# Optimization experiments

Measured on AMD Instinct MI355X. Metric: run time of the kernel, lower is better.

The kernel has to match this reference:

```python
import jax, jax.numpy as jnp
import numpy as np

B, S, H, NH, HD = 2, 2048, 2048, 32, 64
ROPE_THETA = 10000.0


def _rope_tables(seq_len, head_dim, theta):
    inv_freq = 1.0 / (theta ** (jnp.arange(0, head_dim, 2, dtype=jnp.float32) / head_dim))
    t = jnp.arange(seq_len, dtype=jnp.float32)
    freqs = jnp.outer(t, inv_freq)                 # [S, HD/2]
    emb = jnp.concatenate([freqs, freqs], axis=-1)  # [S, HD]
    return jnp.cos(emb), jnp.sin(emb)


def setup_inputs() -> dict:
    key = jax.random.key(0)
    ks = jax.random.split(key, 6)
    cos, sin = _rope_tables(S, HD, ROPE_THETA)
    scale = 0.02
    return {
        "hidden_states": jax.random.normal(ks[0], (B, S, H), dtype=jnp.float32),
        "attention_mask": jnp.zeros((B, S), dtype=jnp.float32),
        "cos": cos,
        "sin": sin,
        "Wq": jax.random.normal(ks[1], (H, H), dtype=jnp.float32) * scale,
        "Wk": jax.random.normal(ks[2], (H, H), dtype=jnp.float32) * scale,
        "Wv": jax.random.normal(ks[3], (H, H), dtype=jnp.float32) * scale,
        "Wo": jax.random.normal(ks[4], (H, H), dtype=jnp.float32) * scale,
    }


def _rotate_half(x):
    x1, x2 = jnp.split(x, 2, axis=-1)
    return jnp.concatenate([-x2, x1], axis=-1)


def reference(hidden_states, attention_mask, cos, sin, Wq, Wk, Wv, Wo):
    b, s, _ = hidden_states.shape
    # QKV projections (nn.Linear: x @ W.T), reshape to [B, NH, S, HD]
    def proj(W):
        y = hidden_states @ W.T
        return y.reshape(b, s, NH, HD).transpose(0, 2, 1, 3)
    q, k, v = proj(Wq), proj(Wk), proj(Wv)
    # RoPE (HF rotate_half convention); cos/sin: [S, HD] -> broadcast [1,1,S,HD]
    c = cos[None, None, :, :]
    sn = sin[None, None, :, :]
    q = q * c + _rotate_half(q) * sn
    k = k * c + _rotate_half(k) * sn
    # attention: [B, NH, S, S]
    scores = jnp.einsum("bhqd,bhkd->bhqk", q, k) / jnp.sqrt(jnp.float32(HD))
    scores = scores + attention_mask[:, None, None, :]
    probs = jax.nn.softmax(scores, axis=-1)
    out = jnp.einsum("bhqk,bhkd->bhqd", probs, v)
    out = out.transpose(0, 2, 1, 3).reshape(b, s, NH * HD)
    return out @ Wo.T
```

## Files before the change

kernel.cpp:

```cpp
#include <hip/hip_runtime.h>
#include <stdint.h>
#include <math.h>

#define NB 2
#define SS 2048
#define HH 2048
#define NHH 32
#define HDD 64
#define MM (NB*SS)

typedef __attribute__((ext_vector_type(8))) short short8;
typedef __attribute__((ext_vector_type(4))) short short4v;
typedef __attribute__((ext_vector_type(4))) float f32x4;

#define GLOBAL_AS const __attribute__((address_space(1))) void*
#define LDS_AS __attribute__((address_space(3))) void*

static __device__ __forceinline__ short rne_bf16(float x) {
    uint32_t u = __builtin_bit_cast(uint32_t, x);
    u += 0x7FFFu + ((u >> 16) & 1u);
    return (short)(u >> 16);
}
static __device__ __forceinline__ float bf16f(short h) {
    return __builtin_bit_cast(float, (uint32_t)((uint16_t)h) << 16);
}
static __device__ __forceinline__ uint32_t pack_bf16_rne(float a, float b) {
    uint32_t ua = __builtin_bit_cast(uint32_t, a);
    uint32_t ub = __builtin_bit_cast(uint32_t, b);
    ua += 0x7FFFu + ((ua >> 16) & 1u);
    ub += 0x7FFFu + ((ub >> 16) & 1u);
    return __builtin_amdgcn_perm(ub, ua, 0x07060302);
}
static __device__ __forceinline__ float fast_exp2(float x) {
    float r;
    asm("v_exp_f32 %0, %1" : "=v"(r) : "v"(x));
    return r;
}

__global__ void __launch_bounds__(256)
k_cvt(const float* __restrict__ in, short* __restrict__ out, int n4) {
    int i = blockIdx.x * blockDim.x + threadIdx.x;
    if (i >= n4) return;
    float4 f = reinterpret_cast<const float4*>(in)[i];
    short4v o;
    o.x = rne_bf16(f.x); o.y = rne_bf16(f.y);
    o.z = rne_bf16(f.z); o.w = rne_bf16(f.w);
    reinterpret_cast<short4v*>(out)[i] = o;
}

__global__ void __launch_bounds__(256)
k_cvt_split(const float* __restrict__ in, short* __restrict__ hi, short* __restrict__ lo, int n4) {
    int i = blockIdx.x * blockDim.x + threadIdx.x;
    if (i >= n4) return;
    float4 f = reinterpret_cast<const float4*>(in)[i];
    short4v h, l;
    h.x = rne_bf16(f.x); l.x = rne_bf16(f.x - bf16f(h.x));
    h.y = rne_bf16(f.y); l.y = rne_bf16(f.y - bf16f(h.y));
    h.z = rne_bf16(f.z); l.z = rne_bf16(f.z - bf16f(h.z));
    h.w = rne_bf16(f.w); l.w = rne_bf16(f.w - bf16f(h.w));
    reinterpret_cast<short4v*>(hi)[i] = h;
    reinterpret_cast<short4v*>(lo)[i] = l;
}

__global__ void __launch_bounds__(256, 2)
k_gemm_qkv(const short* __restrict__ X,
           const short* __restrict__ Wqh, const short* __restrict__ Wkh, const short* __restrict__ Wvh,
           const float* __restrict__ cosT, const float* __restrict__ sinT,
           short* __restrict__ Qr, short* __restrict__ Kr, short* __restrict__ Vt)
{
    __shared__ short lA[128 * 32];
    __shared__ short lBq[128 * 32];
    __shared__ short lBk[128 * 32];
    __shared__ short lBv[128 * 32];
    const int tid = threadIdx.x;
    const int lane = tid & 63;
    const int wave = tid >> 6;
    const int lrow = lane & 15;
    const int quad = lane >> 4;
    const int mblk = blockIdx.y * 128;
    const int nblk = blockIdx.x * 128;
    const int m0 = mblk + (wave >> 1) * 64;
    const int n0 = nblk + (wave & 1) * 64;
    const int mw = (wave >> 1) * 64;
    const int nw = (wave & 1) * 64;

    const int srow = wave * 32 + (lane >> 2);
    const int skc = (lane & 3) * 8;
    const short* gA = X   + (size_t)(mblk + srow) * HH + skc;
    const short* gQ = Wqh + (size_t)(nblk + srow) * HH + skc;
    const short* gK = Wkh + (size_t)(nblk + srow) * HH + skc;
    const short* gV = Wvh + (size_t)(nblk + srow) * HH + skc;
    const int lofs = wave * 1024;

    f32x4 acc[3][4][4];
    #pragma unroll
    for (int z = 0; z < 3; z++)
        #pragma unroll
        for (int i = 0; i < 4; i++)
            #pragma unroll
            for (int j = 0; j < 4; j++) acc[z][i][j] = 0.f;

    #pragma unroll 1
    for (int k0 = 0; k0 < HH; k0 += 32) {
        __syncthreads();
        #pragma unroll
        for (int j = 0; j < 2; j++) {
            size_t go = (size_t)j * 16 * HH + k0;
            int lo = lofs + j * 512;
            __builtin_amdgcn_global_load_lds((GLOBAL_AS)(gA + go), (LDS_AS)(&lA[lo]),  16, 0, 0);
            __builtin_amdgcn_global_load_lds((GLOBAL_AS)(gQ + go), (LDS_AS)(&lBq[lo]), 16, 0, 0);
            __builtin_amdgcn_global_load_lds((GLOBAL_AS)(gK + go), (LDS_AS)(&lBk[lo]), 16, 0, 0);
            __builtin_amdgcn_global_load_lds((GLOBAL_AS)(gV + go), (LDS_AS)(&lBv[lo]), 16, 0, 0);
        }
        __syncthreads();

        short8 a[4];
        #pragma unroll
        for (int mt = 0; mt < 4; mt++)
            a[mt] = *reinterpret_cast<const short8*>(&lA[(mw + mt * 16 + lrow) * 32 + quad * 8]);

        const short* lBz[3] = { lBq, lBk, lBv };
        #pragma unroll
        for (int z = 0; z < 3; z++) {
            short8 b[4];
            #pragma unroll
            for (int nt = 0; nt < 4; nt++)
                b[nt] = *reinterpret_cast<const short8*>(&lBz[z][(nw + nt * 16 + lrow) * 32 + quad * 8]);
            #pragma unroll
            for (int mt = 0; mt < 4; mt++)
                #pragma unroll
                for (int nt = 0; nt < 4; nt++)
                    acc[z][mt][nt] = __builtin_amdgcn_mfma_f32_16x16x32_bf16(a[mt], b[nt], acc[z][mt][nt], 0, 0, 0);
        }
    }

    const float QSCL = 0.18033688011112042f;

    #pragma unroll
    for (int z = 0; z < 3; z++) {
        #pragma unroll
        for (int mt = 0; mt < 4; mt++) {
            #pragma unroll
            for (int r = 0; r < 4; r++) {
                int row = m0 + mt * 16 + quad * 4 + r;
                int b_i = row >> 11;
                int s_i = row & (SS - 1);
                #pragma unroll
                for (int nt = 0; nt < 4; nt++) {
                    int col = n0 + nt * 16 + lrow;
                    int h_i = col >> 6;
                    int d_i = col & 63;
                    float v = acc[z][mt][nt][r];
                    if (z < 2) {
                        float pair = (nt & 2) ? acc[z][mt][nt - 2][r] : -acc[z][mt][nt + 2][r];
                        float c = cosT[s_i * HDD + d_i];
                        float sn = sinT[s_i * HDD + d_i];
                        v = v * c + pair * sn;
                        if (z == 0) v *= QSCL;
                        short* dst = (z == 0) ? Qr : Kr;
                        dst[(((size_t)b_i * NHH + h_i) * SS + s_i) * HDD + d_i] = rne_bf16(v);
                    } else {
                        Vt[(((size_t)b_i * NHH + h_i) * HDD + d_i) * SS + s_i] = rne_bf16(v);
                    }
                }
            }
        }
    }
}

__global__ void __launch_bounds__(256, 2)
k_attn(const short* __restrict__ Qr, const short* __restrict__ Kr, const short* __restrict__ Vt,
       const float* __restrict__ mask,
       short* __restrict__ Ah, short* __restrict__ Al)
{
    __shared__ short plds[4][4096];
    const int lane = threadIdx.x & 63;
    const int wave = threadIdx.x >> 6;
    const int lrow = lane & 15;
    const int quad = lane >> 4;
    const int aofs = lrow & 7;
    const int b = blockIdx.x >> 5;
    const int h = blockIdx.x & 31;
    const int q0w = blockIdx.y * 256 + wave * 64;

    const size_t bh = (size_t)b * NHH + h;
    const short* Qbase = Qr + bh * SS * HDD;
    const short* Kbase = Kr + bh * SS * HDD;
    const short* Vbase = Vt + bh * (size_t)HDD * SS;
    const float* mrow = mask + b * SS;
    char* cb = (char*)&plds[wave][0];

    short8 qf[4][2];
    #pragma unroll
    for (int nt = 0; nt < 4; nt++)
        #pragma unroll
        for (int c = 0; c < 2; c++)
            qf[nt][c] = *reinterpret_cast<const short8*>(
                Qbase + (size_t)(q0w + nt * 16 + lrow) * HDD + c * 32 + quad * 8);

    f32x4 oacc[4][4];
    float l[4];
    #pragma unroll
    for (int i = 0; i < 4; i++) {
        l[i] = 0.f;
        #pragma unroll
        for (int j = 0; j < 4; j++) oacc[i][j] = 0.f;
    }

    const float L2E = 1.44269504f;

    #pragma unroll 1
    for (int k0 = 0; k0 < SS; k0 += 64) {
        short8 kf[4][2];
        #pragma unroll
        for (int kt = 0; kt < 4; kt++)
            #pragma unroll
            for (int c = 0; c < 2; c++)
                kf[kt][c] = *reinterpret_cast<const short8*>(
                    Kbase + (size_t)(k0 + kt * 16 + lrow) * HDD + c * 32 + quad * 8);

        f32x4 sacc[4][4];
        #pragma unroll
        for (int kt = 0; kt < 4; kt++)
            #pragma unroll
            for (int nt = 0; nt < 4; nt++) {
                f32x4 z4 = 0.f;
                z4 = __builtin_amdgcn_mfma_f32_16x16x32_bf16(kf[kt][0], qf[nt][0], z4, 0, 0, 0);
                sacc[kt][nt] = __builtin_amdgcn_mfma_f32_16x16x32_bf16(kf[kt][1], qf[nt][1], z4, 0, 0, 0);
            }

        asm volatile("s_waitcnt lgkmcnt(0)" ::: "memory");

        #pragma unroll
        for (int kt = 0; kt < 4; kt++) {
            float4 mk = *reinterpret_cast<const float4*>(mrow + k0 + kt * 16 + quad * 4);
            float m0v = mk.x * L2E, m1v = mk.y * L2E, m2v = mk.z * L2E, m3v = mk.w * L2E;
            #pragma unroll
            for (int nt = 0; nt < 4; nt++) {
                float p0 = fast_exp2(sacc[kt][nt][0] + m0v);
                float p1 = fast_exp2(sacc[kt][nt][1] + m1v);
                float p2 = fast_exp2(sacc[kt][nt][2] + m2v);
                float p3 = fast_exp2(sacc[kt][nt][3] + m3v);
                l[nt] += (p0 + p1) + (p2 + p3);
                uint2 w;
                w.x = pack_bf16_rne(p0, p1);
                w.y = pack_bf16_rne(p2, p3);
                *reinterpret_cast<uint2*>(
                    cb + (nt * 16 + lrow) * 128 +
                    (((2 * kt + (quad >> 1)) ^ aofs) * 16) + (quad & 1) * 8) = w;
            }
        }

        asm volatile("s_waitcnt lgkmcnt(0)" ::: "memory");

        #pragma unroll
        for (int c = 0; c < 2; c++) {
            short8 pf[4], vf[4];
            #pragma unroll
            for (int mt = 0; mt < 4; mt++)
                pf[mt] = *reinterpret_cast<const short8*>(
                    cb + (mt * 16 + lrow) * 128 + (((4 * c + quad) ^ aofs) * 16));
            #pragma unroll
            for (int dt = 0; dt < 4; dt++)
                vf[dt] = *reinterpret_cast<const short8*>(
                    Vbase + (size_t)(dt * 16 + lrow) * SS + k0 + c * 32 + quad * 8);
            #pragma unroll
            for (int mt = 0; mt < 4; mt++)
                #pragma unroll
                for (int dt = 0; dt < 4; dt++)
                    oacc[mt][dt] = __builtin_amdgcn_mfma_f32_16x16x32_bf16(pf[mt], vf[dt], oacc[mt][dt], 0, 0, 0);
        }
    }

    #pragma unroll
    for (int nt = 0; nt < 4; nt++) {
        l[nt] += __shfl_xor(l[nt], 16, 64);
        l[nt] += __shfl_xor(l[nt], 32, 64);
    }
    float linv[4][4];
    #pragma unroll
    for (int mt = 0; mt < 4; mt++)
        #pragma unroll
        for (int r = 0; r < 4; r++)
            linv[mt][r] = 1.f / __shfl(l[mt], quad * 4 + r, 16);

    #pragma unroll
    for (int mt = 0; mt < 4; mt++) {
        #pragma unroll
        for (int r = 0; r < 4; r++) {
            int s_i = q0w + mt * 16 + quad * 4 + r;
            size_t row = (size_t)b * SS + s_i;
            #pragma unroll
            for (int dt = 0; dt < 4; dt++) {
                float x = oacc[mt][dt][r] * linv[mt][r];
                short hi = rne_bf16(x);
                short lo = rne_bf16(x - bf16f(hi));
                size_t idx = row * HH + (size_t)h * 64 + dt * 16 + lrow;
                Ah[idx] = hi;
                Al[idx] = lo;
            }
        }
    }
}

__global__ void __launch_bounds__(256, 2)
k_gemm_wo(const short* __restrict__ Ahh, const short* __restrict__ All,
          const short* __restrict__ Bhh, const short* __restrict__ Bll,
          float* __restrict__ C)
{
    __shared__ short lAh[128 * 32];
    __shared__ short lAl[128 * 32];
    __shared__ short lBh[128 * 32];
    __shared__ short lBl[128 * 32];
    const int tid = threadIdx.x;
    const int lane = tid & 63;
    const int wave = tid >> 6;
    const int lrow = lane & 15;
    const int quad = lane >> 4;
    const int mblk = blockIdx.y * 128;
    const int nblk = blockIdx.x * 128;
    const int m0 = mblk + (wave >> 1) * 64;
    const int n0 = nblk + (wave & 1) * 64;
    const int mw = (wave >> 1) * 64;
    const int nw = (wave & 1) * 64;

    const int srow = wave * 32 + (lane >> 2);
    const int skc = (lane & 3) * 8;
    const short* gAh = Ahh + (size_t)(mblk + srow) * HH + skc;
    const short* gAl = All + (size_t)(mblk + srow) * HH + skc;
    const short* gBh = Bhh + (size_t)(nblk + srow) * HH + skc;
    const short* gBl = Bll + (size_t)(nblk + srow) * HH + skc;
    short* lAhw = &lAh[wave * 1024];
    short* lAlw = &lAl[wave * 1024];
    short* lBhw = &lBh[wave * 1024];
    short* lBlw = &lBl[wave * 1024];

    f32x4 acc[4][4];
    #pragma unroll
    for (int i = 0; i < 4; i++)
        #pragma unroll
        for (int j = 0; j < 4; j++) acc[i][j] = 0.f;

    #pragma unroll 1
    for (int k0 = 0; k0 < HH; k0 += 32) {
        __syncthreads();
        #pragma unroll
        for (int j = 0; j < 2; j++) {
            size_t go = (size_t)j * 16 * HH + k0;
            __builtin_amdgcn_global_load_lds((GLOBAL_AS)(gAh + go), (LDS_AS)(lAhw + j * 512), 16, 0, 0);
            __builtin_amdgcn_global_load_lds((GLOBAL_AS)(gAl + go), (LDS_AS)(lAlw + j * 512), 16, 0, 0);
            __builtin_amdgcn_global_load_lds((GLOBAL_AS)(gBh + go), (LDS_AS)(lBhw + j * 512), 16, 0, 0);
            __builtin_amdgcn_global_load_lds((GLOBAL_AS)(gBl + go), (LDS_AS)(lBlw + j * 512), 16, 0, 0);
        }
        __syncthreads();

        short8 ah[4], al[4], bh[4], bl[4];
        #pragma unroll
        for (int mt = 0; mt < 4; mt++) {
            int off = (mw + mt * 16 + lrow) * 32 + quad * 8;
            ah[mt] = *reinterpret_cast<const short8*>(&lAh[off]);
            al[mt] = *reinterpret_cast<const short8*>(&lAl[off]);
        }
        #pragma unroll
        for (int nt = 0; nt < 4; nt++) {
            int off = (nw + nt * 16 + lrow) * 32 + quad * 8;
            bh[nt] = *reinterpret_cast<const short8*>(&lBh[off]);
            bl[nt] = *reinterpret_cast<const short8*>(&lBl[off]);
        }
        #pragma unroll
        for (int mt = 0; mt < 4; mt++)
            #pragma unroll
            for (int nt = 0; nt < 4; nt++) {
                acc[mt][nt] = __builtin_amdgcn_mfma_f32_16x16x32_bf16(ah[mt], bh[nt], acc[mt][nt], 0, 0, 0);
                acc[mt][nt] = __builtin_amdgcn_mfma_f32_16x16x32_bf16(al[mt], bh[nt], acc[mt][nt], 0, 0, 0);
                acc[mt][nt] = __builtin_amdgcn_mfma_f32_16x16x32_bf16(ah[mt], bl[nt], acc[mt][nt], 0, 0, 0);
            }
    }

    #pragma unroll
    for (int mt = 0; mt < 4; mt++)
        #pragma unroll
        for (int r = 0; r < 4; r++) {
            int row = m0 + mt * 16 + quad * 4 + r;
            #pragma unroll
            for (int nt = 0; nt < 4; nt++) {
                int col = n0 + nt * 16 + lrow;
                C[(size_t)row * HH + col] = acc[mt][nt][r];
            }
        }
}

extern "C" void kernel_launch(void* const* d_in, const int* in_sizes, int n_in,
                              void* d_out, int out_size, void* d_ws, size_t ws_size,
                              hipStream_t stream) {
    const float* hidden = (const float*)d_in[0];
    const float* maskp  = (const float*)d_in[1];
    const float* cosT   = (const float*)d_in[2];
    const float* sinT   = (const float*)d_in[3];
    const float* Wq     = (const float*)d_in[4];
    const float* Wk     = (const float*)d_in[5];
    const float* Wv     = (const float*)d_in[6];
    const float* Wo     = (const float*)d_in[7];
    float* out = (float*)d_out;

    char* ws = (char*)d_ws;
    auto alloc = [&](size_t bytes) {
        char* p = ws;
        ws += (bytes + 255) & ~(size_t)255;
        return p;
    };
    const size_t XB = (size_t)MM * HH * sizeof(short);
    const size_t WB = (size_t)HH * HH * sizeof(short);
    short* Xh  = (short*)alloc(XB);
    short* Wqh = (short*)alloc(WB);
    short* Wkh = (short*)alloc(WB);
    short* Wvh = (short*)alloc(WB);
    short* Woh = (short*)alloc(WB);
    short* Wol = (short*)alloc(WB);
    short* Qr  = (short*)alloc(XB);
    short* Kr  = (short*)alloc(XB);
    short* Vt  = (short*)alloc(XB);
    short* Ah  = (short*)alloc(XB);
    short* Al  = (short*)alloc(XB);

    const int nX4 = MM * HH / 4;
    const int nW4 = HH * HH / 4;
    k_cvt<<<dim3(nX4 / 256), dim3(256), 0, stream>>>(hidden, Xh, nX4);
    k_cvt<<<dim3(nW4 / 256), dim3(256), 0, stream>>>(Wq, Wqh, nW4);
    k_cvt<<<dim3(nW4 / 256), dim3(256), 0, stream>>>(Wk, Wkh, nW4);
    k_cvt<<<dim3(nW4 / 256), dim3(256), 0, stream>>>(Wv, Wvh, nW4);
    k_cvt_split<<<dim3(nW4 / 256), dim3(256), 0, stream>>>(Wo, Woh, Wol, nW4);

    k_gemm_qkv<<<dim3(HH / 128, MM / 128), dim3(256), 0, stream>>>(
        Xh, Wqh, Wkh, Wvh, cosT, sinT, Qr, Kr, Vt);

    k_attn<<<dim3(NB * NHH, SS / 256), dim3(256), 0, stream>>>(
        Qr, Kr, Vt, maskp, Ah, Al);

    k_gemm_wo<<<dim3(HH / 128, MM / 128), dim3(256), 0, stream>>>(
        Ah, Al, Woh, Wol, out);
}
```

Measured before the change: 494.3 us.

## Software-pipeline attention loop with double-buffered P tile and K prefetch

Double-buffers the per-wave P tile in LDS so each iteration's PV MFMAs consume the previous tile's probabilities while the current tile's exp/pack runs. The K fragments for the next tile are prefetched into registers during the current iteration, and the explicit lgkmcnt waits are removed. The aim is to overlap exp work, LDS traffic and global loads with MFMA issue. In exchange it doubles LDS per block, raises register pressure at 2 waves/EU occupancy, and relies on a zeroed buffer for the first iteration plus an epilogue for the last tile. It also drops the explicit LDS wait before reading P, leaving ordering to the compiler.

```diff
diff --git a/kernel.cpp b/kernel.cpp
--- a/kernel.cpp
+++ b/kernel.cpp
@@ -173,7 +173,7 @@
        const float* __restrict__ mask,
        short* __restrict__ Ah, short* __restrict__ Al)
 {
-    __shared__ short plds[4][4096];
+    __shared__ short plds[4][2][4096];
     const int lane = threadIdx.x & 63;
     const int wave = threadIdx.x >> 6;
     const int lrow = lane & 15;
@@ -188,7 +188,15 @@
     const short* Kbase = Kr + bh * SS * HDD;
     const short* Vbase = Vt + bh * (size_t)HDD * SS;
     const float* mrow = mask + b * SS;
-    char* cb = (char*)&plds[wave][0];
+    char* cb0 = (char*)&plds[wave][0][0];
+    char* cb1 = (char*)&plds[wave][1][0];
+
+    {
+        uint4 z4 = make_uint4(0, 0, 0, 0);
+        #pragma unroll
+        for (int i = 0; i < 8; i++)
+            *reinterpret_cast<uint4*>(cb1 + lane * 128 + i * 16) = z4;
+    }
 
     short8 qf[4][2];
     #pragma unroll
@@ -198,6 +206,14 @@
             qf[nt][c] = *reinterpret_cast<const short8*>(
                 Qbase + (size_t)(q0w + nt * 16 + lrow) * HDD + c * 32 + quad * 8);
 
+    short8 kf[4][2];
+    #pragma unroll
+    for (int kt = 0; kt < 4; kt++)
+        #pragma unroll
+        for (int c = 0; c < 2; c++)
+            kf[kt][c] = *reinterpret_cast<const short8*>(
+                Kbase + (size_t)(kt * 16 + lrow) * HDD + c * 32 + quad * 8);
+
     f32x4 oacc[4][4];
     float l[4];
     #pragma unroll
@@ -211,13 +227,10 @@
 
     #pragma unroll 1
     for (int k0 = 0; k0 < SS; k0 += 64) {
-        short8 kf[4][2];
-        #pragma unroll
-        for (int kt = 0; kt < 4; kt++)
-            #pragma unroll
-            for (int c = 0; c < 2; c++)
-                kf[kt][c] = *reinterpret_cast<const short8*>(
-                    Kbase + (size_t)(k0 + kt * 16 + lrow) * HDD + c * 32 + quad * 8);
+        const int pc = (k0 >> 6) & 1;
+        char* cbw = pc ? cb1 : cb0;
+        char* cbr = pc ? cb0 : cb1;
+        const int kprev = (k0 == 0) ? 0 : k0 - 64;
 
         f32x4 sacc[4][4];
         #pragma unroll
@@ -229,10 +242,18 @@
                 sacc[kt][nt] = __builtin_amdgcn_mfma_f32_16x16x32_bf16(kf[kt][1], qf[nt][1], z4, 0, 0, 0);
             }
 
-        asm volatile("s_waitcnt lgkmcnt(0)" ::: "memory");
-
-        #pragma unroll
-        for (int kt = 0; kt < 4; kt++) {
+        short8 pf0[4], vf0[4];
+        #pragma unroll
+        for (int mt = 0; mt < 4; mt++)
+            pf0[mt] = *reinterpret_cast<const short8*>(
+                cbr + (mt * 16 + lrow) * 128 + ((quad ^ aofs) * 16));
+        #pragma unroll
+        for (int dt = 0; dt < 4; dt++)
+            vf0[dt] = *reinterpret_cast<const short8*>(
+                Vbase + (size_t)(dt * 16 + lrow) * SS + kprev + quad * 8);
+
+        #pragma unroll
+        for (int kt = 0; kt < 2; kt++) {
             float4 mk = *reinterpret_cast<const float4*>(mrow + k0 + kt * 16 + quad * 4);
             float m0v = mk.x * L2E, m1v = mk.y * L2E, m2v = mk.z * L2E, m3v = mk.w * L2E;
             #pragma unroll
@@ -246,24 +267,78 @@
                 w.x = pack_bf16_rne(p0, p1);
                 w.y = pack_bf16_rne(p2, p3);
                 *reinterpret_cast<uint2*>(
-                    cb + (nt * 16 + lrow) * 128 +
+                    cbw + (nt * 16 + lrow) * 128 +
                     (((2 * kt + (quad >> 1)) ^ aofs) * 16) + (quad & 1) * 8) = w;
             }
         }
 
-        asm volatile("s_waitcnt lgkmcnt(0)" ::: "memory");
-
+        #pragma unroll
+        for (int mt = 0; mt < 4; mt++)
+            #pragma unroll
+            for (int dt = 0; dt < 4; dt++)
+                oacc[mt][dt] = __builtin_amdgcn_mfma_f32_16x16x32_bf16(pf0[mt], vf0[dt], oacc[mt][dt], 0, 0, 0);
+
+        {
+            const int kn = (k0 + 64 < SS) ? (k0 + 64) : k0;
+            #pragma unroll
+            for (int kt = 0; kt < 4; kt++)
+                #pragma unroll
+                for (int c = 0; c < 2; c++)
+                    kf[kt][c] = *reinterpret_cast<const short8*>(
+                        Kbase + (size_t)(kn + kt * 16 + lrow) * HDD + c * 32 + quad * 8);
+        }
+
+        short8 pf1[4], vf1[4];
+        #pragma unroll
+        for (int mt = 0; mt < 4; mt++)
+            pf1[mt] = *reinterpret_cast<const short8*>(
+                cbr + (mt * 16 + lrow) * 128 + (((4 + quad) ^ aofs) * 16));
+        #pragma unroll
+        for (int dt = 0; dt < 4; dt++)
+            vf1[dt] = *reinterpret_cast<const short8*>(
+                Vbase + (size_t)(dt * 16 + lrow) * SS + kprev + 32 + quad * 8);
+
+        #pragma unroll
+        for (int kt = 2; kt < 4; kt++) {
+            float4 mk = *reinterpret_cast<const float4*>(mrow + k0 + kt * 16 + quad * 4);
+            float m0v = mk.x * L2E, m1v = mk.y * L2E, m2v = mk.z * L2E, m3v = mk.w * L2E;
+            #pragma unroll
+            for (int nt = 0; nt < 4; nt++) {
+                float p0 = fast_exp2(sacc[kt][nt][0] + m0v);
+                float p1 = fast_exp2(sacc[kt][nt][1] + m1v);
+                float p2 = fast_exp2(sacc[kt][nt][2] + m2v);
+                float p3 = fast_exp2(sacc[kt][nt][3] + m3v);
+                l[nt] += (p0 + p1) + (p2 + p3);
+                uint2 w;
+                w.x = pack_bf16_rne(p0, p1);
+                w.y = pack_bf16_rne(p2, p3);
+                *reinterpret_cast<uint2*>(
+                    cbw + (nt * 16 + lrow) * 128 +
+                    (((2 * kt + (quad >> 1)) ^ aofs) * 16) + (quad & 1) * 8) = w;
+            }
+        }
+
+        #pragma unroll
+        for (int mt = 0; mt < 4; mt++)
+            #pragma unroll
+            for (int dt = 0; dt < 4; dt++)
+                oacc[mt][dt] = __builtin_amdgcn_mfma_f32_16x16x32_bf16(pf1[mt], vf1[dt], oacc[mt][dt], 0, 0, 0);
+    }
+
+    {
+        char* cbr = cb1;
+        const int kprev = SS - 64;
         #pragma unroll
         for (int c = 0; c < 2; c++) {
             short8 pf[4], vf[4];
             #pragma unroll
             for (int mt = 0; mt < 4; mt++)
                 pf[mt] = *reinterpret_cast<const short8*>(
-                    cb + (mt * 16 + lrow) * 128 + (((4 * c + quad) ^ aofs) * 16));
+                    cbr + (mt * 16 + lrow) * 128 + (((4 * c + quad) ^ aofs) * 16));
             #pragma unroll
             for (int dt = 0; dt < 4; dt++)
                 vf[dt] = *reinterpret_cast<const short8*>(
-                    Vbase + (size_t)(dt * 16 + lrow) * SS + k0 + c * 32 + quad * 8);
+                    Vbase + (size_t)(dt * 16 + lrow) * SS + kprev + c * 32 + quad * 8);
             #pragma unroll
             for (int mt = 0; mt < 4; mt++)
                 #pragma unroll
```

Measured after the change: 500.4 us. About the same (+1.2%).
